# Kernel optimization log

Measured on AMD Instinct MI355X. Metric: run time of the kernel, lower is better.

Reference implementation:

```python
import jax, jax.numpy as jnp
import numpy as np

MIN_, MAX_, KSZ, IGNORE_IDX = 10, 10, 3, -255
B, H, W = 256, 256, 256
LI_MAX_ITERS = 64


def setup_inputs() -> dict:
    key = jax.random.key(0)
    x = jax.random.uniform(key, (B, 1, H, W), dtype=jnp.float32)
    return {"x": x}


def _otsu(hist):
    # hist: [256] counts. Returns Otsu threshold (bin value); fg = img > t.
    bins = jnp.arange(256, dtype=jnp.float32)
    w0 = jnp.cumsum(hist)[:-1]
    w1 = hist.sum() - w0
    s0 = jnp.cumsum(hist * bins)[:-1]
    s_tot = (hist * bins).sum()
    m0 = s0 / jnp.maximum(w0, 1e-12)
    m1 = (s_tot - s0) / jnp.maximum(w1, 1e-12)
    var_b = w0 * w1 * (m0 - m1) ** 2
    return jnp.argmax(var_b).astype(jnp.float32)


def _li(hist, init_t):
    # Histogram-based Li iterative minimum cross-entropy threshold
    # (skimage.filters.threshold_li with initial_guess=init_t).
    bins = jnp.arange(256, dtype=jnp.float32)
    img_min = jnp.min(jnp.where(hist > 0, bins, 255.0))
    vals = bins - img_min  # shift so values >= 0 (as skimage does)
    csum = jnp.cumsum(hist)
    cvsum = jnp.cumsum(hist * vals)
    n_tot, s_tot = csum[-1], cvsum[-1]
    tol = 0.5  # integer image -> half the minimal value spacing

    def body(state):
        t_curr, _, i = state
        # background: img <= t_curr + img_min
        idx = jnp.clip(jnp.floor(t_curr + img_min).astype(jnp.int32), 0, 255)
        n_back, s_back = csum[idx], cvsum[idx]
        n_fore, s_fore = n_tot - n_back, s_tot - s_back
        mean_back = jnp.where(n_back > 0, s_back / jnp.maximum(n_back, 1.0), 0.0)
        mean_fore = s_fore / jnp.maximum(n_fore, 1.0)
        eps = 1e-12
        t_next = (mean_back - mean_fore) / (
            jnp.log(jnp.maximum(mean_back, eps)) - jnp.log(jnp.maximum(mean_fore, eps)))
        t_next = jnp.where(mean_back < eps, mean_fore / 2.0, t_next)
        return (t_next, t_curr, i + 1)

    def cond(state):
        t_curr, t_prev, i = state
        return (jnp.abs(t_curr - t_prev) > tol) & (i < LI_MAX_ITERS)

    t0 = init_t - img_min
    t_fin, _, _ = jax.lax.while_loop(cond, body, (t0, t0 + 10.0, 0))
    return t_fin + img_min


def _sample_mask(key, region, k):
    # Uniform sampling without replacement of up to k pixels from region
    # (bool [H,W]) via random-score top-k (equiv. to torch.multinomial
    # with uniform probs, w/o replacement).
    flat = region.reshape(-1)
    scores = jnp.where(flat, jax.random.uniform(key, (flat.shape[0],)), -1.0)
    top, idx = jax.lax.top_k(scores, k)
    valid = (top >= 0.0).astype(jnp.int32)
    mask = jnp.zeros(flat.shape[0], jnp.int32).at[idx].max(valid)
    return mask.reshape(region.shape)


def _dilate(m):
    # kornia dilation with ones (KSZ,KSZ) kernel on a 0/1 mask == max filter.
    return jax.lax.reduce_window(m, 0, jax.lax.max, (KSZ, KSZ), (1, 1), "SAME")


def _per_image(img_u8, key_fg, key_bg):
    # img_u8: [H,W] int32 in [0,255]
    hist = jnp.zeros(256, jnp.float32).at[img_u8.ravel()].add(1.0)
    otsu = jnp.clip(_otsu(hist), 1.0, 254.0)  # clamp 0->1, 255->254
    li_t = _li(hist, otsu)
    roi = img_u8.astype(jnp.float32) > li_t

    fg = _sample_mask(key_fg, roi, MAX_)
    bg = _sample_mask(key_bg, jnp.logical_not(roi), MIN_)
    if KSZ > 1:
        fg = _dilate(fg)
        bg = _dilate(bg)

    overlap = (fg + bg) == 2
    fg = jnp.where(overlap, 0, fg)
    bg = jnp.where(overlap, 0, bg)

    seeds = jnp.full((H, W), IGNORE_IDX, jnp.int32)
    seeds = jnp.where(bg == 1, 0, seeds)
    seeds = jnp.where(fg == 1, 1, seeds)
    return seeds


def reference(x):
    b = x.shape[0]
    # (cam*255).astype(uint8): truncation, cam in [0,1]
    img = jnp.clip(jnp.floor(x[:, 0] * 255.0), 0, 255).astype(jnp.int32)
    keys = jax.random.split(jax.random.key(1), (b, 2))
    return jax.vmap(_per_image)(img, keys[:, 0], keys[:, 1])
```

## Files before the change

### kernel.cpp

```cpp
#include <hip/hip_runtime.h>
#include <stdint.h>

#define NPIX 65536
#define IGN (-255)
#define CAP 768

__device__ __forceinline__ uint32_t rotl32(uint32_t v, uint32_t r){ return (v<<r)|(v>>(32u-r)); }

__device__ __forceinline__ void tf2x32(uint32_t k0, uint32_t k1, uint32_t x0, uint32_t x1,
                                       uint32_t &o0, uint32_t &o1){
  uint32_t k2 = k0 ^ k1 ^ 0x1BD11BDAu;
  x0 += k0; x1 += k1;
#define TFR(r) { x0 += x1; x1 = rotl32(x1,(r)); x1 ^= x0; }
  TFR(13u) TFR(15u) TFR(26u) TFR(6u)   x0 += k1; x1 += k2 + 1u;
  TFR(17u) TFR(29u) TFR(16u) TFR(24u)  x0 += k2; x1 += k0 + 2u;
  TFR(13u) TFR(15u) TFR(26u) TFR(6u)   x0 += k0; x1 += k1 + 3u;
  TFR(17u) TFR(29u) TFR(16u) TFR(24u)  x0 += k1; x1 += k2 + 4u;
  TFR(13u) TFR(15u) TFR(26u) TFR(6u)   x0 += k2; x1 += k0 + 5u;
#undef TFR
  o0 = x0; o1 = x1;
}

__device__ __forceinline__ unsigned long long packCand(uint32_t bits, uint32_t pix){
  float f = __uint_as_float((bits >> 9) | 0x3f800000u) - 1.0f;
  uint32_t u = __float_as_uint(f) ^ 0x80000000u;
  return ((unsigned long long)u << 32) | (unsigned long long)(0xFFFFFFFFu - pix);
}

__device__ __forceinline__ void t10_insert(unsigned long long* l, unsigned long long c){
  if (c > l[9]) {
    l[9] = c;
#pragma unroll
    for (int i = 9; i > 0; --i){
      unsigned long long a = l[i-1], b2 = l[i];
      if (b2 > a){ l[i-1] = b2; l[i] = a; }
    }
  }
}

__global__ __launch_bounds__(1024, 4)
void apm_kernel(const float* __restrict__ x, int* __restrict__ out){
  const int b = blockIdx.x;
  const int tid = threadIdx.x;
  const float* img = x + (size_t)b * NPIX;
  int* outb = out + (size_t)b * NPIX;

  __shared__ uint32_t hist[256];
  __shared__ float csum[256], cvsum[256];
  __shared__ unsigned long long buf[2][CAP];
  __shared__ uint32_t s_kw[4];
  __shared__ int s_cnt[2];
  __shared__ int s_nroi;
  __shared__ int s_imin;
  __shared__ unsigned long long s_best;
  __shared__ float s_lit;
  __shared__ int s_fail[2];
  __shared__ int s_pr[2][10], s_pc[2][10], s_np[2];

  if (tid < 256) hist[tid] = 0u;
  if (tid == 0){ s_cnt[0] = 0; s_cnt[1] = 0; s_nroi = 0; s_imin = 255; s_best = 0ull; }
  if (tid < 2){
    uint32_t o0, o1;
    tf2x32(0u, 1u, 0u, (uint32_t)(2*b + tid), o0, o1);
    s_kw[2*tid] = o0; s_kw[2*tid+1] = o1;
  }
  __syncthreads();

  uint32_t packed[16];
  {
    int4 f4 = make_int4(IGN, IGN, IGN, IGN);
    const float4* x4 = (const float4*)img;
    int4* o4 = (int4*)outb;
#pragma unroll
    for (int j = 0; j < 16; ++j){
      int p4 = tid + 1024*j;
      float4 v = x4[p4];
      o4[p4] = f4;
      uint32_t u0 = (uint32_t)min(max((int)floorf(v.x*255.0f),0),255);
      uint32_t u1 = (uint32_t)min(max((int)floorf(v.y*255.0f),0),255);
      uint32_t u2 = (uint32_t)min(max((int)floorf(v.z*255.0f),0),255);
      uint32_t u3 = (uint32_t)min(max((int)floorf(v.w*255.0f),0),255);
      packed[j] = u0 | (u1<<8) | (u2<<16) | (u3<<24);
      atomicAdd(&hist[u0],1u); atomicAdd(&hist[u1],1u);
      atomicAdd(&hist[u2],1u); atomicAdd(&hist[u3],1u);
    }
  }
  __syncthreads();

  if (tid < 256 && hist[tid]) atomicMin(&s_imin, tid);
  __syncthreads();
  const float img_min = (float)s_imin;

  if (tid < 256){
    float h = (float)hist[tid];
    csum[tid]  = h;
    cvsum[tid] = h * ((float)tid - img_min);
  }
  __syncthreads();
  for (int off = 1; off < 256; off <<= 1){
    float a = 0.f, c2 = 0.f;
    if (tid < 256 && tid >= off){ a = csum[tid-off]; c2 = cvsum[tid-off]; }
    __syncthreads();
    if (tid < 256 && tid >= off){ csum[tid] += a; cvsum[tid] += c2; }
    __syncthreads();
  }

  {
    float s_tot_o = cvsum[255] + img_min * csum[255];
    if (tid < 255){
      float w0 = csum[tid];
      float w1 = 65536.0f - w0;
      float cs = cvsum[tid] + img_min * csum[tid];
      float m0 = cs / fmaxf(w0, 1e-12f);
      float m1 = (s_tot_o - cs) / fmaxf(w1, 1e-12f);
      float d = m0 - m1;
      float vb = (w0*w1) * (d*d);
      unsigned long long pk =
        ((unsigned long long)__float_as_uint(vb) << 32) | (unsigned long long)(255 - tid);
      atomicMax(&s_best, pk);
    }
  }
  __syncthreads();

  if (tid == 0){
    int bestIdx = 255 - (int)(s_best & 0xFFFFFFFFull);
    float otsu = fminf(fmaxf((float)bestIdx, 1.0f), 254.0f);
    float n_tot = csum[255], s_tot = cvsum[255];
    float t_curr = otsu - img_min, t_prev = t_curr + 10.0f;
    int it = 0;
    while (fabsf(t_curr - t_prev) > 0.5f && it < 64){
      int idx = min(max((int)floorf(t_curr + img_min), 0), 255);
      float n_back = csum[idx], s_back = cvsum[idx];
      float n_fore = n_tot - n_back, s_fore = s_tot - s_back;
      float mean_back = (n_back > 0.0f) ? (s_back / fmaxf(n_back, 1.0f)) : 0.0f;
      float mean_fore = s_fore / fmaxf(n_fore, 1.0f);
      float t_next = (mean_back - mean_fore) /
                     (logf(fmaxf(mean_back, 1e-12f)) - logf(fmaxf(mean_fore, 1e-12f)));
      if (mean_back < 1e-12f) t_next = mean_fore * 0.5f;
      t_prev = t_curr; t_curr = t_next; ++it;
    }
    s_lit = t_curr + img_min;
  }
  __syncthreads();

  const float lit = s_lit;
  const uint32_t fk0 = s_kw[0], fk1 = s_kw[1], bk0 = s_kw[2], bk1 = s_kw[3];
  const uint32_t THRM = (0xFF000000u >> 9);
  int my_roi = 0;
#pragma unroll
  for (int j = 0; j < 16; ++j){
    uint32_t pk = packed[j];
    uint32_t pix0 = (uint32_t)(4*(tid + 1024*j));
#pragma unroll
    for (int s = 0; s < 4; ++s){
      uint32_t q = (pk >> (8*s)) & 255u;
      bool r = ((float)q > lit);
      my_roi += r ? 1 : 0;
      uint32_t o0, o1;
      tf2x32(r ? fk0 : bk0, r ? fk1 : bk1, 0u, pix0 + (uint32_t)s, o0, o1);
      uint32_t bits = o0 ^ o1;
      if ((bits >> 9) >= THRM){
        int r2 = r ? 0 : 1;
        int idx = atomicAdd(&s_cnt[r2], 1);
        if (idx < CAP) buf[r2][idx] = packCand(bits, pix0 + (uint32_t)s);
      }
    }
  }
  for (int off = 32; off; off >>= 1) my_roi += __shfl_down(my_roi, off);
  if ((tid & 63) == 0) atomicAdd(&s_nroi, my_roi);
  __syncthreads();

  if (tid == 0){
    int m0r = s_nroi, m1r = NPIX - s_nroi;
    int c0 = s_cnt[0], c1 = s_cnt[1];
    s_fail[0] = (c0 > CAP) || (c0 < 10 && c0 != m0r);
    s_fail[1] = (c1 > CAP) || (c1 < 10 && c1 != m1r);
  }
  __syncthreads();

  if (s_fail[0] || s_fail[1]){
    if (tid < 64){
      for (int r2 = 0; r2 < 2; ++r2){
        if (!s_fail[r2]) continue;
        uint32_t kk0 = s_kw[2*r2], kk1 = s_kw[2*r2+1];
        unsigned long long t[10];
#pragma unroll
        for (int i = 0; i < 10; ++i) t[i] = 0ull;
        for (int k2 = 0; k2 < 1024; ++k2){
          uint32_t pix = (uint32_t)(tid + 64*k2);
          float v = img[pix];
          int q = min(max((int)floorf(v*255.0f),0),255);
          bool r = ((float)q > lit);
          if (r != (r2 == 0)) continue;
          uint32_t o0, o1; tf2x32(kk0, kk1, 0u, pix, o0, o1);
          t10_insert(t, packCand(o0 ^ o1, pix));
        }
#pragma unroll
        for (int i = 0; i < 10; ++i) buf[r2][tid*10 + i] = t[i];
      }
    }
    __syncthreads();
    if (tid < 2 && s_fail[tid]){
      unsigned long long t[10];
#pragma unroll
      for (int i = 0; i < 10; ++i) t[i] = 0ull;
      for (int i = 0; i < 640; ++i) t10_insert(t, buf[tid][i]);
#pragma unroll
      for (int i = 0; i < 10; ++i) buf[tid][i] = t[i];
      s_cnt[tid] = 10;
    }
    __syncthreads();
  }

  if (tid == 0 || tid == 64){
    int r2 = (tid == 0) ? 0 : 1;
    int n = min(s_cnt[r2], CAP);
    unsigned long long t[10];
#pragma unroll
    for (int i = 0; i < 10; ++i) t[i] = 0ull;
    for (int i = 0; i < n; ++i) t10_insert(t, buf[r2][i]);
    int np = 0;
    for (int i = 0; i < 10; ++i){
      if (t[i]){
        uint32_t pix = 0xFFFFFFFFu - (uint32_t)(t[i] & 0xFFFFFFFFull);
        s_pr[r2][np] = (int)(pix >> 8);
        s_pc[r2][np] = (int)(pix & 255u);
        ++np;
      }
    }
    s_np[r2] = np;
  }
  __syncthreads();

  const int nfg = s_np[0], nbg = s_np[1];
  const int npts = nfg + nbg;
  if (tid < npts*9){
    int k = tid / 9, d = tid - k*9;
    int pr = (k < nfg) ? s_pr[0][k] : s_pr[1][k - nfg];
    int pc = (k < nfg) ? s_pc[0][k] : s_pc[1][k - nfg];
    pr += d/3 - 1; pc += d%3 - 1;
    if (pr >= 0 && pr < 256 && pc >= 0 && pc < 256){
      bool fgd = false, bgd = false;
      for (int i = 0; i < nfg; ++i) fgd |= (abs(pr - s_pr[0][i]) <= 1) && (abs(pc - s_pc[0][i]) <= 1);
      for (int i = 0; i < nbg; ++i) bgd |= (abs(pr - s_pr[1][i]) <= 1) && (abs(pc - s_pc[1][i]) <= 1);
      int val = (fgd && bgd) ? IGN : (fgd ? 1 : 0);
      outb[pr*256 + pc] = val;
    }
  }
}

extern "C" void kernel_launch(void* const* d_in, const int* in_sizes, int n_in,
                              void* d_out, int out_size, void* d_ws, size_t ws_size,
                              hipStream_t stream) {
  const float* x = (const float*)d_in[0];
  int* out = (int*)d_out;
  int B = in_sizes[0] / NPIX;
  apm_kernel<<<B, 1024, 0, stream>>>(x, out);
}
```

Baseline: 177.6 us.

## Split per-image work across 8 blocks with global-atomic histogram and last-block reduction

Replaces the single 1024-thread block per image with three kernels: a workspace init, a histogram pass where 8 blocks per image each cover a chunk and merge histograms via global atomics (the last-finishing block computes Otsu/Li thresholds), and a scoring pass where 8 blocks per image generate threefry candidates into global buffers with a last-block top-k and dilation. The aim is more blocks than the 256 of the original, so all CUs are filled and load latency is hidden. The cost is reading the input twice, extra launches, global atomics and threadfence handoffs. It also adds a sub-banked shared histogram, nontemporal fill stores and an integer threshold cut.

```diff
diff --git a/kernel.cpp b/kernel.cpp
--- a/kernel.cpp
+++ b/kernel.cpp
@@ -3,7 +3,20 @@
 
 #define NPIX 65536
 #define IGN (-255)
-#define CAP 768
+#define CAP 256
+#define SPLIT 8
+
+typedef unsigned long long u64;
+typedef int v4i __attribute__((ext_vector_type(4)));
+
+#define WS_HIST   0
+#define WS_LIT    65536
+#define WS_ROI    65792
+#define WS_DONE1  66048
+#define WS_DONE2  66304
+#define WS_CNT    66560
+#define WS_U32_END 67072
+#define WS_CAND_BYTE 268288
 
 __device__ __forceinline__ uint32_t rotl32(uint32_t v, uint32_t r){ return (v<<r)|(v>>(32u-r)); }
 
@@ -21,107 +34,110 @@
   o0 = x0; o1 = x1;
 }
 
-__device__ __forceinline__ unsigned long long packCand(uint32_t bits, uint32_t pix){
+__device__ __forceinline__ uint32_t tf_bits(uint32_t k0, uint32_t k1, uint32_t k2, uint32_t pix){
+  uint32_t x0 = k0, x1 = pix + k1;
+#define TFR(r) { x0 += x1; x1 = rotl32(x1,(r)); x1 ^= x0; }
+  TFR(13u) TFR(15u) TFR(26u) TFR(6u)   x0 += k1; x1 += k2 + 1u;
+  TFR(17u) TFR(29u) TFR(16u) TFR(24u)  x0 += k2; x1 += k0 + 2u;
+  TFR(13u) TFR(15u) TFR(26u) TFR(6u)   x0 += k0; x1 += k1 + 3u;
+  TFR(17u) TFR(29u) TFR(16u) TFR(24u)  x0 += k1; x1 += k2 + 4u;
+  TFR(13u) TFR(15u) TFR(26u) TFR(6u)   x0 += k2; x1 += k0 + 5u;
+#undef TFR
+  return x0 ^ x1;
+}
+
+__device__ __forceinline__ u64 packCand(uint32_t bits, uint32_t pix){
   float f = __uint_as_float((bits >> 9) | 0x3f800000u) - 1.0f;
   uint32_t u = __float_as_uint(f) ^ 0x80000000u;
-  return ((unsigned long long)u << 32) | (unsigned long long)(0xFFFFFFFFu - pix);
-}
-
-__device__ __forceinline__ void t10_insert(unsigned long long* l, unsigned long long c){
+  return ((u64)u << 32) | (u64)(0xFFFFFFFFu - pix);
+}
+
+__device__ __forceinline__ void t10_insert(u64* l, u64 c){
   if (c > l[9]) {
     l[9] = c;
 #pragma unroll
     for (int i = 9; i > 0; --i){
-      unsigned long long a = l[i-1], b2 = l[i];
+      u64 a = l[i-1], b2 = l[i];
       if (b2 > a){ l[i-1] = b2; l[i] = a; }
     }
   }
 }
 
-__global__ __launch_bounds__(1024, 4)
-void apm_kernel(const float* __restrict__ x, int* __restrict__ out){
-  const int b = blockIdx.x;
+__global__ void k0_init(uint32_t* __restrict__ ws){
+  int i = blockIdx.x*1024 + threadIdx.x;
+  if (i < WS_U32_END) ws[i] = 0u;
+}
+
+__global__ __launch_bounds__(256)
+void k1_hist(const float* __restrict__ x, int* __restrict__ out, uint32_t* __restrict__ ws){
+  const int img = blockIdx.x >> 3;
+  const int chk = blockIdx.x & 7;
   const int tid = threadIdx.x;
-  const float* img = x + (size_t)b * NPIX;
-  int* outb = out + (size_t)b * NPIX;
-
-  __shared__ uint32_t hist[256];
+  const float4* x4 = (const float4*)(x + (size_t)img * NPIX);
+  v4i* o4 = (v4i*)(out + (size_t)img * NPIX);
+
+  __shared__ uint32_t h4[1024];
   __shared__ float csum[256], cvsum[256];
-  __shared__ unsigned long long buf[2][CAP];
-  __shared__ uint32_t s_kw[4];
-  __shared__ int s_cnt[2];
-  __shared__ int s_nroi;
-  __shared__ int s_imin;
-  __shared__ unsigned long long s_best;
-  __shared__ float s_lit;
-  __shared__ int s_fail[2];
-  __shared__ int s_pr[2][10], s_pc[2][10], s_np[2];
-
-  if (tid < 256) hist[tid] = 0u;
-  if (tid == 0){ s_cnt[0] = 0; s_cnt[1] = 0; s_nroi = 0; s_imin = 255; s_best = 0ull; }
-  if (tid < 2){
-    uint32_t o0, o1;
-    tf2x32(0u, 1u, 0u, (uint32_t)(2*b + tid), o0, o1);
-    s_kw[2*tid] = o0; s_kw[2*tid+1] = o1;
-  }
-  __syncthreads();
-
-  uint32_t packed[16];
-  {
-    int4 f4 = make_int4(IGN, IGN, IGN, IGN);
-    const float4* x4 = (const float4*)img;
-    int4* o4 = (int4*)outb;
-#pragma unroll
-    for (int j = 0; j < 16; ++j){
-      int p4 = tid + 1024*j;
-      float4 v = x4[p4];
-      o4[p4] = f4;
-      uint32_t u0 = (uint32_t)min(max((int)floorf(v.x*255.0f),0),255);
-      uint32_t u1 = (uint32_t)min(max((int)floorf(v.y*255.0f),0),255);
-      uint32_t u2 = (uint32_t)min(max((int)floorf(v.z*255.0f),0),255);
-      uint32_t u3 = (uint32_t)min(max((int)floorf(v.w*255.0f),0),255);
-      packed[j] = u0 | (u1<<8) | (u2<<16) | (u3<<24);
-      atomicAdd(&hist[u0],1u); atomicAdd(&hist[u1],1u);
-      atomicAdd(&hist[u2],1u); atomicAdd(&hist[u3],1u);
-    }
-  }
-  __syncthreads();
-
-  if (tid < 256 && hist[tid]) atomicMin(&s_imin, tid);
+  __shared__ u64 s_best;
+  __shared__ int s_imin, s_old;
+
+  h4[tid] = 0u; h4[tid+256] = 0u; h4[tid+512] = 0u; h4[tid+768] = 0u;
+  __syncthreads();
+
+  const int sub = tid & 3;
+  const v4i f4 = {IGN, IGN, IGN, IGN};
+#pragma unroll
+  for (int j = 0; j < 8; ++j){
+    int p4 = chk*2048 + j*256 + tid;
+    float4 v = x4[p4];
+    __builtin_nontemporal_store(f4, &o4[p4]);
+    uint32_t q0 = (uint32_t)min(max((int)floorf(v.x*255.0f),0),255);
+    uint32_t q1 = (uint32_t)min(max((int)floorf(v.y*255.0f),0),255);
+    uint32_t q2 = (uint32_t)min(max((int)floorf(v.z*255.0f),0),255);
+    uint32_t q3 = (uint32_t)min(max((int)floorf(v.w*255.0f),0),255);
+    atomicAdd(&h4[q0*4+sub],1u); atomicAdd(&h4[q1*4+sub],1u);
+    atomicAdd(&h4[q2*4+sub],1u); atomicAdd(&h4[q3*4+sub],1u);
+  }
+  __syncthreads();
+  uint32_t hsum = h4[tid*4] + h4[tid*4+1] + h4[tid*4+2] + h4[tid*4+3];
+  if (hsum) atomicAdd(&ws[WS_HIST + img*256 + tid], hsum);
+  __threadfence();
+  __syncthreads();
+  if (tid == 0) s_old = (int)atomicAdd(&ws[WS_DONE1 + img], 1u);
+  __syncthreads();
+  if (s_old != SPLIT-1) return;
+
+  __threadfence();
+  uint32_t h = atomicAdd(&ws[WS_HIST + img*256 + tid], 0u);
+  if (tid == 0){ s_imin = 255; s_best = 0ull; }
+  __syncthreads();
+  if (h) atomicMin(&s_imin, tid);
   __syncthreads();
   const float img_min = (float)s_imin;
-
-  if (tid < 256){
-    float h = (float)hist[tid];
-    csum[tid]  = h;
-    cvsum[tid] = h * ((float)tid - img_min);
-  }
+  csum[tid]  = (float)h;
+  cvsum[tid] = (float)h * ((float)tid - img_min);
   __syncthreads();
   for (int off = 1; off < 256; off <<= 1){
     float a = 0.f, c2 = 0.f;
-    if (tid < 256 && tid >= off){ a = csum[tid-off]; c2 = cvsum[tid-off]; }
+    if (tid >= off){ a = csum[tid-off]; c2 = cvsum[tid-off]; }
     __syncthreads();
-    if (tid < 256 && tid >= off){ csum[tid] += a; cvsum[tid] += c2; }
+    if (tid >= off){ csum[tid] += a; cvsum[tid] += c2; }
     __syncthreads();
   }
-
   {
     float s_tot_o = cvsum[255] + img_min * csum[255];
     if (tid < 255){
-      float w0 = csum[tid];
-      float w1 = 65536.0f - w0;
+      float w0 = csum[tid], w1 = 65536.0f - w0;
       float cs = cvsum[tid] + img_min * csum[tid];
       float m0 = cs / fmaxf(w0, 1e-12f);
       float m1 = (s_tot_o - cs) / fmaxf(w1, 1e-12f);
       float d = m0 - m1;
       float vb = (w0*w1) * (d*d);
-      unsigned long long pk =
-        ((unsigned long long)__float_as_uint(vb) << 32) | (unsigned long long)(255 - tid);
+      u64 pk = ((u64)__float_as_uint(vb) << 32) | (u64)(255 - tid);
       atomicMax(&s_best, pk);
     }
   }
   __syncthreads();
-
   if (tid == 0){
     int bestIdx = 255 - (int)(s_best & 0xFFFFFFFFull);
     float otsu = fminf(fmaxf((float)bestIdx, 1.0f), 254.0f);
@@ -139,99 +155,141 @@
       if (mean_back < 1e-12f) t_next = mean_fore * 0.5f;
       t_prev = t_curr; t_curr = t_next; ++it;
     }
-    s_lit = t_curr + img_min;
-  }
-  __syncthreads();
-
-  const float lit = s_lit;
+    float lit = t_curr + img_min;
+    ws[WS_LIT + img] = __float_as_uint(lit);
+    int qcut = (int)floorf(lit) + 1;
+    uint32_t nroi;
+    if (qcut <= 0)        nroi = NPIX;
+    else if (qcut > 255)  nroi = 0u;
+    else                  nroi = NPIX - (uint32_t)csum[qcut-1];
+    ws[WS_ROI + img] = nroi;
+  }
+}
+
+__global__ __launch_bounds__(256)
+void k2_score(const float* __restrict__ x, int* __restrict__ out,
+              uint32_t* __restrict__ ws, u64* __restrict__ cand){
+  const int img = blockIdx.x >> 3;
+  const int chk = blockIdx.x & 7;
+  const int tid = threadIdx.x;
+  const float4* x4 = (const float4*)(x + (size_t)img * NPIX);
+
+  __shared__ uint32_t s_kw[4];
+  __shared__ int s_old;
+  __shared__ u64 smem[640];
+  __shared__ u64 s_top[2][10];
+  __shared__ int s_fail[2], s_pr[2][10], s_pc[2][10], s_np[2];
+
+  if (tid < 2){
+    uint32_t o0, o1;
+    tf2x32(0u, 1u, 0u, (uint32_t)(2*img + tid), o0, o1);
+    s_kw[2*tid] = o0; s_kw[2*tid+1] = o1;
+  }
+  __syncthreads();
+  const float lit = __uint_as_float(ws[WS_LIT + img]);
+  const int qcut = (int)floorf(lit) + 1;
   const uint32_t fk0 = s_kw[0], fk1 = s_kw[1], bk0 = s_kw[2], bk1 = s_kw[3];
-  const uint32_t THRM = (0xFF000000u >> 9);
-  int my_roi = 0;
-#pragma unroll
-  for (int j = 0; j < 16; ++j){
-    uint32_t pk = packed[j];
-    uint32_t pix0 = (uint32_t)(4*(tid + 1024*j));
+  const uint32_t fk2 = fk0 ^ fk1 ^ 0x1BD11BDAu;
+  const uint32_t bk2 = bk0 ^ bk1 ^ 0x1BD11BDAu;
+  u64* c0p = cand + ((size_t)img*2 + 0)*CAP;
+  u64* c1p = cand + ((size_t)img*2 + 1)*CAP;
+
+#pragma unroll
+  for (int j = 0; j < 8; ++j){
+    int p4 = chk*2048 + j*256 + tid;
+    float4 v = x4[p4];
+    uint32_t pix0 = (uint32_t)(p4*4);
+    float vv[4] = {v.x, v.y, v.z, v.w};
 #pragma unroll
     for (int s = 0; s < 4; ++s){
-      uint32_t q = (pk >> (8*s)) & 255u;
-      bool r = ((float)q > lit);
-      my_roi += r ? 1 : 0;
-      uint32_t o0, o1;
-      tf2x32(r ? fk0 : bk0, r ? fk1 : bk1, 0u, pix0 + (uint32_t)s, o0, o1);
-      uint32_t bits = o0 ^ o1;
-      if ((bits >> 9) >= THRM){
+      int q = min(max((int)floorf(vv[s]*255.0f),0),255);
+      bool r = (q >= qcut);
+      uint32_t bits = tf_bits(r?fk0:bk0, r?fk1:bk1, r?fk2:bk2, pix0 + (uint32_t)s);
+      if (bits >= 0xFF000000u){
         int r2 = r ? 0 : 1;
-        int idx = atomicAdd(&s_cnt[r2], 1);
-        if (idx < CAP) buf[r2][idx] = packCand(bits, pix0 + (uint32_t)s);
-      }
-    }
-  }
-  for (int off = 32; off; off >>= 1) my_roi += __shfl_down(my_roi, off);
-  if ((tid & 63) == 0) atomicAdd(&s_nroi, my_roi);
-  __syncthreads();
-
+        uint32_t idx = atomicAdd(&ws[WS_CNT + img*2 + r2], 1u);
+        if (idx < CAP) atomicExch((r2 ? c1p : c0p) + idx, packCand(bits, pix0 + (uint32_t)s));
+      }
+    }
+  }
+  __threadfence();
+  __syncthreads();
+  if (tid == 0) s_old = (int)atomicAdd(&ws[WS_DONE2 + img], 1u);
+  __syncthreads();
+  if (s_old != SPLIT-1) return;
+
+  __threadfence();
+  const uint32_t nroi = ws[WS_ROI + img];
+  int c0 = (int)atomicAdd(&ws[WS_CNT + img*2 + 0], 0u);
+  int c1 = (int)atomicAdd(&ws[WS_CNT + img*2 + 1], 0u);
   if (tid == 0){
-    int m0r = s_nroi, m1r = NPIX - s_nroi;
-    int c0 = s_cnt[0], c1 = s_cnt[1];
-    s_fail[0] = (c0 > CAP) || (c0 < 10 && c0 != m0r);
-    s_fail[1] = (c1 > CAP) || (c1 < 10 && c1 != m1r);
-  }
-  __syncthreads();
-
-  if (s_fail[0] || s_fail[1]){
-    if (tid < 64){
-      for (int r2 = 0; r2 < 2; ++r2){
-        if (!s_fail[r2]) continue;
-        uint32_t kk0 = s_kw[2*r2], kk1 = s_kw[2*r2+1];
-        unsigned long long t[10];
+    s_fail[0] = (c0 > CAP) || (c0 < 10 && c0 != (int)nroi);
+    s_fail[1] = (c1 > CAP) || (c1 < 10 && c1 != (int)(NPIX - nroi));
+  }
+  __syncthreads();
+
+  for (int r2 = 0; r2 < 2; ++r2){
+    int cc = (r2 ? c1 : c0);
+    if (!s_fail[r2]){
+      int n = min(cc, CAP);
+      if (tid < n) smem[tid] = atomicAdd((r2 ? c1p : c0p) + tid, 0ull);
+      __syncthreads();
+      if (tid == 0){
+        u64 t[10];
 #pragma unroll
         for (int i = 0; i < 10; ++i) t[i] = 0ull;
-        for (int k2 = 0; k2 < 1024; ++k2){
-          uint32_t pix = (uint32_t)(tid + 64*k2);
-          float v = img[pix];
+        for (int i = 0; i < n; ++i) t10_insert(t, smem[i]);
+#pragma unroll
+        for (int i = 0; i < 10; ++i) s_top[r2][i] = t[i];
+      }
+      __syncthreads();
+    } else {
+      if (tid < 64){
+        uint32_t kk0 = s_kw[2*r2], kk1 = s_kw[2*r2+1], kk2 = kk0 ^ kk1 ^ 0x1BD11BDAu;
+        u64 t[10];
+#pragma unroll
+        for (int i = 0; i < 10; ++i) t[i] = 0ull;
+        for (int k = 0; k < 1024; ++k){
+          uint32_t pix = (uint32_t)(tid + 64*k);
+          float v = x[(size_t)img*NPIX + pix];
           int q = min(max((int)floorf(v*255.0f),0),255);
-          bool r = ((float)q > lit);
-          if (r != (r2 == 0)) continue;
-          uint32_t o0, o1; tf2x32(kk0, kk1, 0u, pix, o0, o1);
-          t10_insert(t, packCand(o0 ^ o1, pix));
+          bool r = (q >= qcut);
+          if (r == (r2 == 0)){
+            t10_insert(t, packCand(tf_bits(kk0, kk1, kk2, pix), pix));
+          }
         }
 #pragma unroll
-        for (int i = 0; i < 10; ++i) buf[r2][tid*10 + i] = t[i];
-      }
-    }
-    __syncthreads();
-    if (tid < 2 && s_fail[tid]){
-      unsigned long long t[10];
-#pragma unroll
-      for (int i = 0; i < 10; ++i) t[i] = 0ull;
-      for (int i = 0; i < 640; ++i) t10_insert(t, buf[tid][i]);
-#pragma unroll
-      for (int i = 0; i < 10; ++i) buf[tid][i] = t[i];
-      s_cnt[tid] = 10;
-    }
-    __syncthreads();
-  }
-
-  if (tid == 0 || tid == 64){
-    int r2 = (tid == 0) ? 0 : 1;
-    int n = min(s_cnt[r2], CAP);
-    unsigned long long t[10];
-#pragma unroll
-    for (int i = 0; i < 10; ++i) t[i] = 0ull;
-    for (int i = 0; i < n; ++i) t10_insert(t, buf[r2][i]);
+        for (int i = 0; i < 10; ++i) smem[tid*10 + i] = t[i];
+      }
+      __syncthreads();
+      if (tid == 0){
+        u64 t[10];
+#pragma unroll
+        for (int i = 0; i < 10; ++i) t[i] = 0ull;
+        for (int i = 0; i < 640; ++i) t10_insert(t, smem[i]);
+#pragma unroll
+        for (int i = 0; i < 10; ++i) s_top[r2][i] = t[i];
+      }
+      __syncthreads();
+    }
+  }
+
+  if (tid < 2){
     int np = 0;
     for (int i = 0; i < 10; ++i){
-      if (t[i]){
-        uint32_t pix = 0xFFFFFFFFu - (uint32_t)(t[i] & 0xFFFFFFFFull);
-        s_pr[r2][np] = (int)(pix >> 8);
-        s_pc[r2][np] = (int)(pix & 255u);
+      u64 e = s_top[tid][i];
+      if (e){
+        uint32_t pix = 0xFFFFFFFFu - (uint32_t)(e & 0xFFFFFFFFull);
+        s_pr[tid][np] = (int)(pix >> 8);
+        s_pc[tid][np] = (int)(pix & 255u);
         ++np;
       }
     }
-    s_np[r2] = np;
-  }
-  __syncthreads();
-
+    s_np[tid] = np;
+  }
+  __syncthreads();
+
+  int* outb = out + (size_t)img * NPIX;
   const int nfg = s_np[0], nbg = s_np[1];
   const int npts = nfg + nbg;
   if (tid < npts*9){
@@ -254,6 +312,11 @@
                               hipStream_t stream) {
   const float* x = (const float*)d_in[0];
   int* out = (int*)d_out;
+  uint32_t* ws = (uint32_t*)d_ws;
+  u64* cand = (u64*)((char*)d_ws + WS_CAND_BYTE);
   int B = in_sizes[0] / NPIX;
-  apm_kernel<<<B, 1024, 0, stream>>>(x, out);
-}
+
+  k0_init<<<(WS_U32_END + 1023)/1024, 1024, 0, stream>>>(ws);
+  k1_hist<<<B*SPLIT, 256, 0, stream>>>(x, out, ws);
+  k2_score<<<B*SPLIT, 256, 0, stream>>>(x, out, ws, cand);
+}
```

New measurement: 667.8 us. 3.76x slower.

## Split fused per-image kernel into three multi-block kernels via workspace

Applied to the files above, without the earlier changes.

Replaces the single 1024-thread block per image with three kernels. The first builds partial histograms over 8 chunks per image, using sub-binned shared histograms and nontemporal output fill. The second recomputes Otsu/Li per chunk and generates per-chunk random candidates. The third merges candidates and writes the dilated seeds. The aim is more blocks and better occupancy than 256 heavy blocks, at the cost of extra launches, workspace traffic, and redundant threshold computation in each chunk. The original fused kernel is kept as a fallback when the workspace is too small.

```diff
diff --git a/kernel.cpp b/kernel.cpp
--- a/kernel.cpp
+++ b/kernel.cpp
@@ -3,7 +3,10 @@
 
 #define NPIX 65536
 #define IGN (-255)
-#define CAP 768
+#define CAPB 96
+
+typedef unsigned long long u64;
+typedef int v4i __attribute__((ext_vector_type(4)));
 
 __device__ __forceinline__ uint32_t rotl32(uint32_t v, uint32_t r){ return (v<<r)|(v>>(32u-r)); }
 
@@ -21,107 +24,120 @@
   o0 = x0; o1 = x1;
 }
 
-__device__ __forceinline__ unsigned long long packCand(uint32_t bits, uint32_t pix){
+__device__ __forceinline__ uint32_t tf_bits(uint32_t k0, uint32_t k1, uint32_t k2, uint32_t pix){
+  uint32_t x0 = k0, x1 = pix + k1;
+#define TFR(r) { x0 += x1; x1 = rotl32(x1,(r)); x1 ^= x0; }
+  TFR(13u) TFR(15u) TFR(26u) TFR(6u)   x0 += k1; x1 += k2 + 1u;
+  TFR(17u) TFR(29u) TFR(16u) TFR(24u)  x0 += k2; x1 += k0 + 2u;
+  TFR(13u) TFR(15u) TFR(26u) TFR(6u)   x0 += k0; x1 += k1 + 3u;
+  TFR(17u) TFR(29u) TFR(16u) TFR(24u)  x0 += k1; x1 += k2 + 4u;
+  TFR(13u) TFR(15u) TFR(26u) TFR(6u)   x0 += k2; x1 += k0 + 5u;
+#undef TFR
+  return x0 ^ x1;
+}
+
+__device__ __forceinline__ u64 packCand(uint32_t bits, uint32_t pix){
   float f = __uint_as_float((bits >> 9) | 0x3f800000u) - 1.0f;
   uint32_t u = __float_as_uint(f) ^ 0x80000000u;
-  return ((unsigned long long)u << 32) | (unsigned long long)(0xFFFFFFFFu - pix);
-}
-
-__device__ __forceinline__ void t10_insert(unsigned long long* l, unsigned long long c){
+  return ((u64)u << 32) | (u64)(0xFFFFFFFFu - pix);
+}
+
+__device__ __forceinline__ void t10_insert(u64* l, u64 c){
   if (c > l[9]) {
     l[9] = c;
 #pragma unroll
     for (int i = 9; i > 0; --i){
-      unsigned long long a = l[i-1], b2 = l[i];
+      u64 a = l[i-1], b2 = l[i];
       if (b2 > a){ l[i-1] = b2; l[i] = a; }
     }
   }
 }
 
-__global__ __launch_bounds__(1024, 4)
-void apm_kernel(const float* __restrict__ x, int* __restrict__ out){
-  const int b = blockIdx.x;
+__global__ __launch_bounds__(256)
+void k1_hist(const float* __restrict__ x, int* __restrict__ out,
+             uint32_t* __restrict__ phist, uint32_t* __restrict__ u8c, int use_u8){
+  const int img = blockIdx.x >> 3;
+  const int chk = blockIdx.x & 7;
   const int tid = threadIdx.x;
-  const float* img = x + (size_t)b * NPIX;
-  int* outb = out + (size_t)b * NPIX;
-
-  __shared__ uint32_t hist[256];
+  const float4* x4 = (const float4*)(x + (size_t)img * NPIX);
+  v4i* o4 = (v4i*)(out + (size_t)img * NPIX);
+
+  __shared__ uint32_t h4[1024];
+  h4[tid] = 0u; h4[tid+256] = 0u; h4[tid+512] = 0u; h4[tid+768] = 0u;
+  __syncthreads();
+
+  const int sub = tid & 3;
+  const v4i f4 = {IGN, IGN, IGN, IGN};
+#pragma unroll
+  for (int j = 0; j < 8; ++j){
+    int p4 = chk*2048 + j*256 + tid;
+    float4 v = x4[p4];
+    __builtin_nontemporal_store(f4, &o4[p4]);
+    uint32_t q0 = (uint32_t)min(max((int)floorf(v.x*255.0f),0),255);
+    uint32_t q1 = (uint32_t)min(max((int)floorf(v.y*255.0f),0),255);
+    uint32_t q2 = (uint32_t)min(max((int)floorf(v.z*255.0f),0),255);
+    uint32_t q3 = (uint32_t)min(max((int)floorf(v.w*255.0f),0),255);
+    if (use_u8) u8c[(size_t)img*16384 + p4] = q0 | (q1<<8) | (q2<<16) | (q3<<24);
+    atomicAdd(&h4[q0*4+sub],1u); atomicAdd(&h4[q1*4+sub],1u);
+    atomicAdd(&h4[q2*4+sub],1u); atomicAdd(&h4[q3*4+sub],1u);
+  }
+  __syncthreads();
+  phist[(size_t)(img*8+chk)*256 + tid] = h4[tid*4] + h4[tid*4+1] + h4[tid*4+2] + h4[tid*4+3];
+}
+
+__global__ __launch_bounds__(256)
+void k2_score(const float* __restrict__ x, const uint32_t* __restrict__ u8c,
+              const uint32_t* __restrict__ phist, uint32_t* __restrict__ qcutp,
+              uint32_t* __restrict__ nroip, uint32_t* __restrict__ bcnt,
+              u64* __restrict__ cand, int use_u8){
+  const int img = blockIdx.x >> 3;
+  const int chk = blockIdx.x & 7;
+  const int tid = threadIdx.x;
+
   __shared__ float csum[256], cvsum[256];
-  __shared__ unsigned long long buf[2][CAP];
-  __shared__ uint32_t s_kw[4];
-  __shared__ int s_cnt[2];
-  __shared__ int s_nroi;
-  __shared__ int s_imin;
-  __shared__ unsigned long long s_best;
-  __shared__ float s_lit;
-  __shared__ int s_fail[2];
-  __shared__ int s_pr[2][10], s_pc[2][10], s_np[2];
-
-  if (tid < 256) hist[tid] = 0u;
-  if (tid == 0){ s_cnt[0] = 0; s_cnt[1] = 0; s_nroi = 0; s_imin = 255; s_best = 0ull; }
+  __shared__ u64 s_best;
+  __shared__ int s_imin, s_qcut;
+  __shared__ uint32_t s_kw[4], s_cnt[2];
+  __shared__ u64 s_cand[2][CAPB];
+
   if (tid < 2){
     uint32_t o0, o1;
-    tf2x32(0u, 1u, 0u, (uint32_t)(2*b + tid), o0, o1);
+    tf2x32(0u, 1u, 0u, (uint32_t)(2*img + tid), o0, o1);
     s_kw[2*tid] = o0; s_kw[2*tid+1] = o1;
   }
-  __syncthreads();
-
-  uint32_t packed[16];
-  {
-    int4 f4 = make_int4(IGN, IGN, IGN, IGN);
-    const float4* x4 = (const float4*)img;
-    int4* o4 = (int4*)outb;
-#pragma unroll
-    for (int j = 0; j < 16; ++j){
-      int p4 = tid + 1024*j;
-      float4 v = x4[p4];
-      o4[p4] = f4;
-      uint32_t u0 = (uint32_t)min(max((int)floorf(v.x*255.0f),0),255);
-      uint32_t u1 = (uint32_t)min(max((int)floorf(v.y*255.0f),0),255);
-      uint32_t u2 = (uint32_t)min(max((int)floorf(v.z*255.0f),0),255);
-      uint32_t u3 = (uint32_t)min(max((int)floorf(v.w*255.0f),0),255);
-      packed[j] = u0 | (u1<<8) | (u2<<16) | (u3<<24);
-      atomicAdd(&hist[u0],1u); atomicAdd(&hist[u1],1u);
-      atomicAdd(&hist[u2],1u); atomicAdd(&hist[u3],1u);
-    }
-  }
-  __syncthreads();
-
-  if (tid < 256 && hist[tid]) atomicMin(&s_imin, tid);
+  if (tid == 0){ s_imin = 255; s_best = 0ull; s_cnt[0] = 0u; s_cnt[1] = 0u; }
+
+  uint32_t h = 0;
+#pragma unroll
+  for (int k = 0; k < 8; ++k) h += phist[(size_t)(img*8+k)*256 + tid];
+  __syncthreads();
+  if (h) atomicMin(&s_imin, tid);
   __syncthreads();
   const float img_min = (float)s_imin;
-
-  if (tid < 256){
-    float h = (float)hist[tid];
-    csum[tid]  = h;
-    cvsum[tid] = h * ((float)tid - img_min);
-  }
+  csum[tid]  = (float)h;
+  cvsum[tid] = (float)h * ((float)tid - img_min);
   __syncthreads();
   for (int off = 1; off < 256; off <<= 1){
     float a = 0.f, c2 = 0.f;
-    if (tid < 256 && tid >= off){ a = csum[tid-off]; c2 = cvsum[tid-off]; }
-    __syncthreads();
-    if (tid < 256 && tid >= off){ csum[tid] += a; cvsum[tid] += c2; }
-    __syncthreads();
-  }
-
+    if (tid >= off){ a = csum[tid-off]; c2 = cvsum[tid-off]; }
+    __syncthreads();
+    if (tid >= off){ csum[tid] += a; cvsum[tid] += c2; }
+    __syncthreads();
+  }
   {
     float s_tot_o = cvsum[255] + img_min * csum[255];
     if (tid < 255){
-      float w0 = csum[tid];
-      float w1 = 65536.0f - w0;
+      float w0 = csum[tid], w1 = 65536.0f - w0;
       float cs = cvsum[tid] + img_min * csum[tid];
       float m0 = cs / fmaxf(w0, 1e-12f);
       float m1 = (s_tot_o - cs) / fmaxf(w1, 1e-12f);
       float d = m0 - m1;
       float vb = (w0*w1) * (d*d);
-      unsigned long long pk =
-        ((unsigned long long)__float_as_uint(vb) << 32) | (unsigned long long)(255 - tid);
+      u64 pk = ((u64)__float_as_uint(vb) << 32) | (u64)(255 - tid);
       atomicMax(&s_best, pk);
     }
   }
   __syncthreads();
-
   if (tid == 0){
     int bestIdx = 255 - (int)(s_best & 0xFFFFFFFFull);
     float otsu = fminf(fmaxf((float)bestIdx, 1.0f), 254.0f);
@@ -139,99 +155,163 @@
       if (mean_back < 1e-12f) t_next = mean_fore * 0.5f;
       t_prev = t_curr; t_curr = t_next; ++it;
     }
-    s_lit = t_curr + img_min;
-  }
-  __syncthreads();
-
-  const float lit = s_lit;
+    float lit = t_curr + img_min;
+    int qcut = (int)floorf(lit) + 1;
+    s_qcut = qcut;
+    if (chk == 0){
+      uint32_t nroi;
+      if (qcut <= 0)        nroi = NPIX;
+      else if (qcut > 255)  nroi = 0u;
+      else                  nroi = NPIX - (uint32_t)csum[qcut-1];
+      qcutp[img] = (uint32_t)qcut;
+      nroip[img] = nroi;
+    }
+  }
+  __syncthreads();
+
+  const int qcut = s_qcut;
   const uint32_t fk0 = s_kw[0], fk1 = s_kw[1], bk0 = s_kw[2], bk1 = s_kw[3];
-  const uint32_t THRM = (0xFF000000u >> 9);
-  int my_roi = 0;
-#pragma unroll
-  for (int j = 0; j < 16; ++j){
-    uint32_t pk = packed[j];
-    uint32_t pix0 = (uint32_t)(4*(tid + 1024*j));
+  const uint32_t fk2 = fk0 ^ fk1 ^ 0x1BD11BDAu;
+  const uint32_t bk2 = bk0 ^ bk1 ^ 0x1BD11BDAu;
+#pragma unroll
+  for (int j = 0; j < 8; ++j){
+    int p4 = chk*2048 + j*256 + tid;
+    uint32_t w;
+    if (use_u8){
+      w = u8c[(size_t)img*16384 + p4];
+    } else {
+      float4 v = ((const float4*)(x + (size_t)img*NPIX))[p4];
+      uint32_t q0 = (uint32_t)min(max((int)floorf(v.x*255.0f),0),255);
+      uint32_t q1 = (uint32_t)min(max((int)floorf(v.y*255.0f),0),255);
+      uint32_t q2 = (uint32_t)min(max((int)floorf(v.z*255.0f),0),255);
+      uint32_t q3 = (uint32_t)min(max((int)floorf(v.w*255.0f),0),255);
+      w = q0 | (q1<<8) | (q2<<16) | (q3<<24);
+    }
+    uint32_t pix0 = (uint32_t)(p4*4);
 #pragma unroll
     for (int s = 0; s < 4; ++s){
-      uint32_t q = (pk >> (8*s)) & 255u;
-      bool r = ((float)q > lit);
-      my_roi += r ? 1 : 0;
-      uint32_t o0, o1;
-      tf2x32(r ? fk0 : bk0, r ? fk1 : bk1, 0u, pix0 + (uint32_t)s, o0, o1);
-      uint32_t bits = o0 ^ o1;
-      if ((bits >> 9) >= THRM){
+      int q = (int)((w >> (8*s)) & 255u);
+      bool r = (q >= qcut);
+      uint32_t bits = tf_bits(r?fk0:bk0, r?fk1:bk1, r?fk2:bk2, pix0 + (uint32_t)s);
+      if (bits >= 0xFF000000u){
         int r2 = r ? 0 : 1;
-        int idx = atomicAdd(&s_cnt[r2], 1);
-        if (idx < CAP) buf[r2][idx] = packCand(bits, pix0 + (uint32_t)s);
+        uint32_t idx = atomicAdd(&s_cnt[r2], 1u);
+        if (idx < CAPB) s_cand[r2][idx] = packCand(bits, pix0 + (uint32_t)s);
       }
     }
   }
-  for (int off = 32; off; off >>= 1) my_roi += __shfl_down(my_roi, off);
-  if ((tid & 63) == 0) atomicAdd(&s_nroi, my_roi);
-  __syncthreads();
-
+  __syncthreads();
+  if (tid < 2) bcnt[(size_t)(img*8+chk)*2 + tid] = s_cnt[tid];
+  {
+    int s = tid >> 7, idx = tid & 127;
+    int n = min((int)s_cnt[s], CAPB);
+    if (idx < n) cand[((size_t)(img*8+chk)*2 + s)*CAPB + idx] = s_cand[s][idx];
+  }
+}
+
+__global__ __launch_bounds__(256)
+void k3_final(const float* __restrict__ x, int* __restrict__ out,
+              const uint32_t* __restrict__ qcutp, const uint32_t* __restrict__ nroip,
+              const uint32_t* __restrict__ bcnt, const u64* __restrict__ cand){
+  const int img = blockIdx.x;
+  const int tid = threadIdx.x;
+
+  __shared__ u64 sbuf[2560];
+  __shared__ u64 s_top[2][10];
+  __shared__ int s_off[2][9], s_fail[2];
+  __shared__ uint32_t s_kw[4];
+  __shared__ int s_pr[2][10], s_pc[2][10], s_np[2];
+
+  if (tid < 2){
+    uint32_t o0, o1;
+    tf2x32(0u, 1u, 0u, (uint32_t)(2*img + tid), o0, o1);
+    s_kw[2*tid] = o0; s_kw[2*tid+1] = o1;
+  }
   if (tid == 0){
-    int m0r = s_nroi, m1r = NPIX - s_nroi;
-    int c0 = s_cnt[0], c1 = s_cnt[1];
-    s_fail[0] = (c0 > CAP) || (c0 < 10 && c0 != m0r);
-    s_fail[1] = (c1 > CAP) || (c1 < 10 && c1 != m1r);
-  }
-  __syncthreads();
-
-  if (s_fail[0] || s_fail[1]){
-    if (tid < 64){
-      for (int r2 = 0; r2 < 2; ++r2){
-        if (!s_fail[r2]) continue;
-        uint32_t kk0 = s_kw[2*r2], kk1 = s_kw[2*r2+1];
-        unsigned long long t[10];
-#pragma unroll
-        for (int i = 0; i < 10; ++i) t[i] = 0ull;
-        for (int k2 = 0; k2 < 1024; ++k2){
-          uint32_t pix = (uint32_t)(tid + 64*k2);
-          float v = img[pix];
-          int q = min(max((int)floorf(v*255.0f),0),255);
-          bool r = ((float)q > lit);
-          if (r != (r2 == 0)) continue;
-          uint32_t o0, o1; tf2x32(kk0, kk1, 0u, pix, o0, o1);
-          t10_insert(t, packCand(o0 ^ o1, pix));
-        }
-#pragma unroll
-        for (int i = 0; i < 10; ++i) buf[r2][tid*10 + i] = t[i];
+    uint32_t nroi = nroip[img];
+    for (int s = 0; s < 2; ++s){
+      int off = 0, fail = 0;
+      for (int k = 0; k < 8; ++k){
+        uint32_t raw = bcnt[(size_t)(img*8+k)*2 + s];
+        if (raw > (uint32_t)CAPB) fail = 1;
+        int ck = (int)min(raw, (uint32_t)CAPB);
+        s_off[s][k] = off; off += ck;
       }
-    }
-    __syncthreads();
-    if (tid < 2 && s_fail[tid]){
-      unsigned long long t[10];
+      s_off[s][8] = off;
+      int region = s ? (int)(NPIX - nroi) : (int)nroi;
+      if (off < 10 && off != region) fail = 1;
+      s_fail[s] = fail;
+    }
+  }
+  __syncthreads();
+
+  {
+    int s = tid >> 7, idx = tid & 127;
+#pragma unroll
+    for (int k = 0; k < 8; ++k){
+      int ck = s_off[s][k+1] - s_off[s][k];
+      if (idx < ck) sbuf[s*1280 + s_off[s][k] + idx] = cand[((size_t)(img*8+k)*2 + s)*CAPB + idx];
+    }
+  }
+  __syncthreads();
+  if (tid == 0 || tid == 128){
+    int s = tid >> 7;
+    if (!s_fail[s]){
+      u64 t[10];
 #pragma unroll
       for (int i = 0; i < 10; ++i) t[i] = 0ull;
-      for (int i = 0; i < 640; ++i) t10_insert(t, buf[tid][i]);
-#pragma unroll
-      for (int i = 0; i < 10; ++i) buf[tid][i] = t[i];
-      s_cnt[tid] = 10;
-    }
-    __syncthreads();
-  }
-
-  if (tid == 0 || tid == 64){
-    int r2 = (tid == 0) ? 0 : 1;
-    int n = min(s_cnt[r2], CAP);
-    unsigned long long t[10];
+      int n = s_off[s][8];
+      for (int i = 0; i < n; ++i) t10_insert(t, sbuf[s*1280 + i]);
+#pragma unroll
+      for (int i = 0; i < 10; ++i) s_top[s][i] = t[i];
+    }
+  }
+  __syncthreads();
+
+  const int qcut = (int)qcutp[img];
+  for (int s = 0; s < 2; ++s){
+    if (!s_fail[s]) continue;
+    uint32_t kk0 = s_kw[2*s], kk1 = s_kw[2*s+1], kk2 = kk0 ^ kk1 ^ 0x1BD11BDAu;
+    u64 t[10];
 #pragma unroll
     for (int i = 0; i < 10; ++i) t[i] = 0ull;
-    for (int i = 0; i < n; ++i) t10_insert(t, buf[r2][i]);
+    for (int k = 0; k < 256; ++k){
+      uint32_t pix = (uint32_t)(tid + 256*k);
+      float v = x[(size_t)img*NPIX + pix];
+      int q = min(max((int)floorf(v*255.0f),0),255);
+      bool r = (q >= qcut);
+      if (r == (s == 0)) t10_insert(t, packCand(tf_bits(kk0, kk1, kk2, pix), pix));
+    }
+#pragma unroll
+    for (int i = 0; i < 10; ++i) sbuf[tid*10 + i] = t[i];
+    __syncthreads();
+    if (tid == 0){
+      u64 m[10];
+#pragma unroll
+      for (int i = 0; i < 10; ++i) m[i] = 0ull;
+      for (int i = 0; i < 2560; ++i) t10_insert(m, sbuf[i]);
+#pragma unroll
+      for (int i = 0; i < 10; ++i) s_top[s][i] = m[i];
+    }
+    __syncthreads();
+  }
+
+  if (tid < 2){
     int np = 0;
     for (int i = 0; i < 10; ++i){
-      if (t[i]){
-        uint32_t pix = 0xFFFFFFFFu - (uint32_t)(t[i] & 0xFFFFFFFFull);
-        s_pr[r2][np] = (int)(pix >> 8);
-        s_pc[r2][np] = (int)(pix & 255u);
+      u64 e = s_top[tid][i];
+      if (e){
+        uint32_t pix = 0xFFFFFFFFu - (uint32_t)(e & 0xFFFFFFFFull);
+        s_pr[tid][np] = (int)(pix >> 8);
+        s_pc[tid][np] = (int)(pix & 255u);
         ++np;
       }
     }
-    s_np[r2] = np;
-  }
-  __syncthreads();
-
+    s_np[tid] = np;
+  }
+  __syncthreads();
+
+  int* outb = out + (size_t)img * NPIX;
   const int nfg = s_np[0], nbg = s_np[1];
   const int npts = nfg + nbg;
   if (tid < npts*9){
@@ -249,11 +329,240 @@
   }
 }
 
+__global__ __launch_bounds__(1024, 4)
+void apm_fused(const float* __restrict__ x, int* __restrict__ out){
+  const int b = blockIdx.x;
+  const int tid = threadIdx.x;
+  const float* img = x + (size_t)b * NPIX;
+  int* outb = out + (size_t)b * NPIX;
+
+  __shared__ uint32_t hist[256];
+  __shared__ float csum[256], cvsum[256];
+  __shared__ u64 buf[2][256];
+  __shared__ uint32_t s_kw[4];
+  __shared__ int s_cnt[2];
+  __shared__ int s_nroi, s_imin;
+  __shared__ u64 s_best;
+  __shared__ float s_lit;
+  __shared__ int s_fail[2];
+  __shared__ int s_pr[2][10], s_pc[2][10], s_np[2];
+
+  if (tid < 256) hist[tid] = 0u;
+  if (tid == 0){ s_cnt[0] = 0; s_cnt[1] = 0; s_nroi = 0; s_imin = 255; s_best = 0ull; }
+  if (tid < 2){
+    uint32_t o0, o1;
+    tf2x32(0u, 1u, 0u, (uint32_t)(2*b + tid), o0, o1);
+    s_kw[2*tid] = o0; s_kw[2*tid+1] = o1;
+  }
+  __syncthreads();
+
+  uint32_t packed[16];
+  {
+    v4i f4 = {IGN, IGN, IGN, IGN};
+    const float4* x4 = (const float4*)img;
+    v4i* o4 = (v4i*)outb;
+#pragma unroll
+    for (int j = 0; j < 16; ++j){
+      int p4 = tid + 1024*j;
+      float4 v = x4[p4];
+      o4[p4] = f4;
+      uint32_t u0 = (uint32_t)min(max((int)floorf(v.x*255.0f),0),255);
+      uint32_t u1 = (uint32_t)min(max((int)floorf(v.y*255.0f),0),255);
+      uint32_t u2 = (uint32_t)min(max((int)floorf(v.z*255.0f),0),255);
+      uint32_t u3 = (uint32_t)min(max((int)floorf(v.w*255.0f),0),255);
+      packed[j] = u0 | (u1<<8) | (u2<<16) | (u3<<24);
+      atomicAdd(&hist[u0],1u); atomicAdd(&hist[u1],1u);
+      atomicAdd(&hist[u2],1u); atomicAdd(&hist[u3],1u);
+    }
+  }
+  __syncthreads();
+  if (tid < 256 && hist[tid]) atomicMin(&s_imin, tid);
+  __syncthreads();
+  const float img_min = (float)s_imin;
+  if (tid < 256){
+    float h = (float)hist[tid];
+    csum[tid]  = h;
+    cvsum[tid] = h * ((float)tid - img_min);
+  }
+  __syncthreads();
+  for (int off = 1; off < 256; off <<= 1){
+    float a = 0.f, c2 = 0.f;
+    if (tid < 256 && tid >= off){ a = csum[tid-off]; c2 = cvsum[tid-off]; }
+    __syncthreads();
+    if (tid < 256 && tid >= off){ csum[tid] += a; cvsum[tid] += c2; }
+    __syncthreads();
+  }
+  {
+    float s_tot_o = cvsum[255] + img_min * csum[255];
+    if (tid < 255){
+      float w0 = csum[tid], w1 = 65536.0f - w0;
+      float cs = cvsum[tid] + img_min * csum[tid];
+      float m0 = cs / fmaxf(w0, 1e-12f);
+      float m1 = (s_tot_o - cs) / fmaxf(w1, 1e-12f);
+      float d = m0 - m1;
+      float vb = (w0*w1) * (d*d);
+      u64 pk = ((u64)__float_as_uint(vb) << 32) | (u64)(255 - tid);
+      atomicMax(&s_best, pk);
+    }
+  }
+  __syncthreads();
+  if (tid == 0){
+    int bestIdx = 255 - (int)(s_best & 0xFFFFFFFFull);
+    float otsu = fminf(fmaxf((float)bestIdx, 1.0f), 254.0f);
+    float n_tot = csum[255], s_tot = cvsum[255];
+    float t_curr = otsu - img_min, t_prev = t_curr + 10.0f;
+    int it = 0;
+    while (fabsf(t_curr - t_prev) > 0.5f && it < 64){
+      int idx = min(max((int)floorf(t_curr + img_min), 0), 255);
+      float n_back = csum[idx], s_back = cvsum[idx];
+      float n_fore = n_tot - n_back, s_fore = s_tot - s_back;
+      float mean_back = (n_back > 0.0f) ? (s_back / fmaxf(n_back, 1.0f)) : 0.0f;
+      float mean_fore = s_fore / fmaxf(n_fore, 1.0f);
+      float t_next = (mean_back - mean_fore) /
+                     (logf(fmaxf(mean_back, 1e-12f)) - logf(fmaxf(mean_fore, 1e-12f)));
+      if (mean_back < 1e-12f) t_next = mean_fore * 0.5f;
+      t_prev = t_curr; t_curr = t_next; ++it;
+    }
+    s_lit = t_curr + img_min;
+  }
+  __syncthreads();
+
+  const float lit = s_lit;
+  const uint32_t fk0 = s_kw[0], fk1 = s_kw[1], bk0 = s_kw[2], bk1 = s_kw[3];
+  const uint32_t THRM = (0xFF000000u >> 9);
+  int my_roi = 0;
+#pragma unroll
+  for (int j = 0; j < 16; ++j){
+    uint32_t pk = packed[j];
+    uint32_t pix0 = (uint32_t)(4*(tid + 1024*j));
+#pragma unroll
+    for (int s = 0; s < 4; ++s){
+      uint32_t q = (pk >> (8*s)) & 255u;
+      bool r = ((float)q > lit);
+      my_roi += r ? 1 : 0;
+      uint32_t o0, o1;
+      tf2x32(r ? fk0 : bk0, r ? fk1 : bk1, 0u, pix0 + (uint32_t)s, o0, o1);
+      uint32_t bits = o0 ^ o1;
+      if ((bits >> 9) >= THRM){
+        int r2 = r ? 0 : 1;
+        int idx = atomicAdd(&s_cnt[r2], 1);
+        if (idx < 256) buf[r2][idx] = packCand(bits, pix0 + (uint32_t)s);
+      }
+    }
+  }
+  for (int off = 32; off; off >>= 1) my_roi += __shfl_down(my_roi, off);
+  if ((tid & 63) == 0) atomicAdd(&s_nroi, my_roi);
+  __syncthreads();
+
+  if (tid == 0){
+    int m0r = s_nroi, m1r = NPIX - s_nroi;
+    int c0 = s_cnt[0], c1 = s_cnt[1];
+    s_fail[0] = (c0 > 256) || (c0 < 10 && c0 != m0r);
+    s_fail[1] = (c1 > 256) || (c1 < 10 && c1 != m1r);
+  }
+  __syncthreads();
+
+  if (s_fail[0] || s_fail[1]){
+    __shared__ u64 smem[640];
+    if (tid < 64){
+      for (int r2 = 0; r2 < 2; ++r2){
+        if (!s_fail[r2]) continue;
+        uint32_t kk0 = s_kw[2*r2], kk1 = s_kw[2*r2+1];
+        u64 t[10];
+#pragma unroll
+        for (int i = 0; i < 10; ++i) t[i] = 0ull;
+        for (int k2 = 0; k2 < 1024; ++k2){
+          uint32_t pix = (uint32_t)(tid + 64*k2);
+          float v = img[pix];
+          int q = min(max((int)floorf(v*255.0f),0),255);
+          bool r = ((float)q > lit);
+          if (r != (r2 == 0)) continue;
+          uint32_t o0, o1; tf2x32(kk0, kk1, 0u, pix, o0, o1);
+          t10_insert(t, packCand(o0 ^ o1, pix));
+        }
+#pragma unroll
+        for (int i = 0; i < 10; ++i) smem[tid*10 + i] = t[i];
+      }
+    }
+    __syncthreads();
+    if (tid < 2 && s_fail[tid]){
+      u64 t[10];
+#pragma unroll
+      for (int i = 0; i < 10; ++i) t[i] = 0ull;
+      for (int i = 0; i < 640; ++i) t10_insert(t, smem[i]);
+#pragma unroll
+      for (int i = 0; i < 10; ++i) buf[tid][i] = t[i];
+      s_cnt[tid] = 10;
+    }
+    __syncthreads();
+  }
+
+  if (tid == 0 || tid == 64){
+    int r2 = (tid == 0) ? 0 : 1;
+    int n = min(s_cnt[r2], 256);
+    u64 t[10];
+#pragma unroll
+    for (int i = 0; i < 10; ++i) t[i] = 0ull;
+    for (int i = 0; i < n; ++i) t10_insert(t, buf[r2][i]);
+    int np = 0;
+    for (int i = 0; i < 10; ++i){
+      if (t[i]){
+        uint32_t pix = 0xFFFFFFFFu - (uint32_t)(t[i] & 0xFFFFFFFFull);
+        s_pr[r2][np] = (int)(pix >> 8);
+        s_pc[r2][np] = (int)(pix & 255u);
+        ++np;
+      }
+    }
+    s_np[r2] = np;
+  }
+  __syncthreads();
+
+  const int nfg = s_np[0], nbg = s_np[1];
+  const int npts = nfg + nbg;
+  if (tid < npts*9){
+    int k = tid / 9, d = tid - k*9;
+    int pr = (k < nfg) ? s_pr[0][k] : s_pr[1][k - nfg];
+    int pc = (k < nfg) ? s_pc[0][k] : s_pc[1][k - nfg];
+    pr += d/3 - 1; pc += d%3 - 1;
+    if (pr >= 0 && pr < 256 && pc >= 0 && pc < 256){
+      bool fgd = false, bgd = false;
+      for (int i = 0; i < nfg; ++i) fgd |= (abs(pr - s_pr[0][i]) <= 1) && (abs(pc - s_pc[0][i]) <= 1);
+      for (int i = 0; i < nbg; ++i) bgd |= (abs(pr - s_pr[1][i]) <= 1) && (abs(pc - s_pc[1][i]) <= 1);
+      int val = (fgd && bgd) ? IGN : (fgd ? 1 : 0);
+      outb[pr*256 + pc] = val;
+    }
+  }
+}
+
 extern "C" void kernel_launch(void* const* d_in, const int* in_sizes, int n_in,
                               void* d_out, int out_size, void* d_ws, size_t ws_size,
                               hipStream_t stream) {
   const float* x = (const float*)d_in[0];
   int* out = (int*)d_out;
   int B = in_sizes[0] / NPIX;
-  apm_kernel<<<B, 1024, 0, stream>>>(x, out);
-}
+
+  size_t cand_b  = (size_t)B * 8 * 2 * CAPB * 8;
+  size_t phist_b = (size_t)B * 8 * 256 * 4;
+  size_t qcut_b  = (size_t)B * 4;
+  size_t nroi_b  = (size_t)B * 4;
+  size_t bcnt_b  = (size_t)B * 8 * 2 * 4;
+  size_t base_need = cand_b + phist_b + qcut_b + nroi_b + bcnt_b;
+  size_t u8_b = (size_t)B * 16384 * 4;
+
+  if (ws_size < base_need){
+    apm_fused<<<B, 1024, 0, stream>>>(x, out);
+    return;
+  }
+  char* p = (char*)d_ws;
+  u64*      cand  = (u64*)p;      p += cand_b;
+  uint32_t* phist = (uint32_t*)p; p += phist_b;
+  uint32_t* qcutp = (uint32_t*)p; p += qcut_b;
+  uint32_t* nroip = (uint32_t*)p; p += nroi_b;
+  uint32_t* bcnt  = (uint32_t*)p; p += bcnt_b;
+  uint32_t* u8c   = (uint32_t*)p;
+  int use_u8 = (ws_size >= base_need + u8_b) ? 1 : 0;
+
+  k1_hist <<<B*8, 256, 0, stream>>>(x, out, phist, u8c, use_u8);
+  k2_score<<<B*8, 256, 0, stream>>>(x, u8c, phist, qcutp, nroip, bcnt, cand, use_u8);
+  k3_final<<<B,   256, 0, stream>>>(x, out, qcutp, nroip, bcnt, cand);
+}
```

Measured after the change: 200.7 us. +13.0%, slower.
